# Kernel optimization log

Measured on AMD Instinct MI355X. Metric: run time of the kernel, lower is better.

Reference implementation:

```python
import jax, jax.numpy as jnp
import numpy as np

N_NODES = 100000
N_EDGES = 600000
IN_CH = 128
HID = 128
N_CLASSES = 2
N_GRAPHS = 64


def setup_inputs() -> dict:
    key = jax.random.key(0)
    ks = jax.random.split(key, 12)
    x = jax.random.normal(ks[0], (N_NODES, IN_CH), dtype=jnp.float32)
    edge_index = jax.random.randint(ks[1], (2, N_EDGES), 0, N_NODES, dtype=jnp.int64)
    batch = jnp.sort(jax.random.randint(ks[2], (N_NODES,), 0, N_GRAPHS, dtype=jnp.int64))
    # GCNConv weights (glorot-ish scale) and biases
    def w(k, fan_in, fan_out):
        return jax.random.normal(k, (fan_in, fan_out), dtype=jnp.float32) / np.sqrt(fan_in)
    return {
        "x": x,
        "edge_index": edge_index,
        "batch": batch,
        "W1": w(ks[3], IN_CH, HID), "b1": jnp.zeros((HID,), jnp.float32),
        "W2": w(ks[4], HID, HID), "b2": jnp.zeros((HID,), jnp.float32),
        "W3": w(ks[5], HID, HID), "b3": jnp.zeros((HID,), jnp.float32),
        "Wl": w(ks[6], HID, N_CLASSES), "bl": jnp.zeros((N_CLASSES,), jnp.float32),
    }


def _gcn_conv(x, W, b, row, col, dinv_sqrt):
    # PyG GCNConv: h = x @ W; add self-loops; symmetric norm; scatter-add; + bias
    h = x @ W  # [N, F]
    norm = dinv_sqrt[row] * dinv_sqrt[col]  # [E]
    msg = norm[:, None] * h[row]  # gather + scale, [E, F]
    out = jnp.zeros_like(h).at[col].add(msg)  # scatter-add to destinations
    out = out + (dinv_sqrt * dinv_sqrt)[:, None] * h  # self-loop term (norm = 1/deg)
    return out + b


def reference(x, edge_index, batch, W1, b1, W2, b2, W3, b3, Wl, bl):
    row, col = edge_index[0], edge_index[1]
    # degree with self-loops (in-degree on col, as in PyG default flow)
    deg = jnp.zeros((N_NODES,), jnp.float32).at[col].add(1.0) + 1.0
    dinv_sqrt = jax.lax.rsqrt(deg)

    h = jax.nn.relu(_gcn_conv(x, W1, b1, row, col, dinv_sqrt))
    h = jax.nn.relu(_gcn_conv(h, W2, b2, row, col, dinv_sqrt))
    h = _gcn_conv(h, W3, b3, row, col, dinv_sqrt)

    # global mean pool over graphs
    sums = jax.ops.segment_sum(h, batch, num_segments=N_GRAPHS)  # [G, F]
    counts = jax.ops.segment_sum(jnp.ones((N_NODES,), jnp.float32), batch, num_segments=N_GRAPHS)
    pooled = sums / jnp.maximum(counts, 1.0)[:, None]

    # dropout p=0.0 is identity; final linear head
    return pooled @ Wl + bl
```

## Files before the change

### kernel.cpp

```cpp
#include <hip/hip_runtime.h>

#define NN 100000
#define NE 600000
#define NG 64
#define FD 128
#define NB 98
#define EPAD 1300000
#define GEMM_BLOCKS 512

typedef __attribute__((ext_vector_type(8))) short s8v;
typedef __attribute__((ext_vector_type(4))) float f4v;

__device__ inline float bflo(unsigned u) { return __uint_as_float(u << 16); }
__device__ inline float bfhi(unsigned u) { return __uint_as_float(u & 0xFFFF0000u); }
__device__ inline unsigned f2bfbits(float f) {
  unsigned x = __float_as_uint(f);
  return (x + 0x7FFFu + ((x >> 16) & 1u)) >> 16;
}
__device__ inline unsigned pack2(float a, float b) { return f2bfbits(a) | (f2bfbits(b) << 16); }

__global__ void k_prep(const int* __restrict__ col, int* __restrict__ counts,
                       const float* __restrict__ W1, const float* __restrict__ W2,
                       const float* __restrict__ W3, unsigned short* __restrict__ WTh,
                       unsigned short* __restrict__ WTl, float* __restrict__ psum,
                       const int* __restrict__ batch, int* __restrict__ starts,
                       int* __restrict__ ends) {
  int tid = blockIdx.x * 256 + threadIdx.x;
  if (tid < NE) atomicAdd(&counts[col[tid]], 1);
  if (tid < NG * FD) psum[tid] = 0.f;
  if (tid < 3 * FD * FD) {
    int which = tid / (FD * FD);
    int r = tid - which * (FD * FD);
    const float* W = which == 0 ? W1 : (which == 1 ? W2 : W3);
    int k = r >> 7, n = r & 127;
    float v = W[r];
    unsigned hb = f2bfbits(v);
    float hf = __uint_as_float(hb << 16);
    unsigned lb = f2bfbits(v - hf);
    WTh[which * FD * FD + n * FD + k] = (unsigned short)hb;
    WTl[which * FD * FD + n * FD + k] = (unsigned short)lb;
  }
  int n = tid;
  if (n >= NN) return;
  int g = batch[n];
  if (n == 0) {
    starts[g] = 0;
    for (int q = 0; q < g; ++q) { starts[q] = 0; ends[q] = 0; }
  } else {
    int gp = batch[n - 1];
    if (gp != g) {
      ends[gp] = n;
      starts[g] = n;
      for (int q = gp + 1; q < g; ++q) { starts[q] = n; ends[q] = n; }
    }
  }
  if (n == NN - 1) {
    ends[g] = NN;
    for (int q = g + 1; q < NG; ++q) { starts[q] = NN; ends[q] = NN; }
  }
}

__global__ void k_bsum(const int* __restrict__ counts, int* __restrict__ bsum,
                       float* __restrict__ dinv) {
  __shared__ int wsm[16];
  int b = blockIdx.x, t = threadIdx.x;
  int i = b * 1024 + t;
  int c = (i < NN) ? counts[i] : 0;
  if (i < NN) dinv[i] = rsqrtf((float)c + 1.0f);
  int x = (i < NN) ? ((c + 7) & ~7) : 0;
#pragma unroll
  for (int d = 32; d; d >>= 1) x += __shfl_down(x, d);
  if ((t & 63) == 0) wsm[t >> 6] = x;
  __syncthreads();
  if (t < 16) {
    int s = wsm[t];
#pragma unroll
    for (int d = 8; d; d >>= 1) s += __shfl_down(s, d);
    if (t == 0) bsum[b] = s;
  }
}

__global__ void k_scan2(const int* __restrict__ counts, const int* __restrict__ bsum,
                        int* __restrict__ indptr) {
  __shared__ int wsm[16];
  __shared__ int s_eb;
  int b = blockIdx.x, t = threadIdx.x;
  int i = b * 1024 + t;
  int lane = t & 63, wid = t >> 6;

  if (wid == 0) {
    int s = 0;
    if (lane < NB && lane < b) s += bsum[lane];
    int l2 = lane + 64;
    if (l2 < NB && l2 < b) s += bsum[l2];
#pragma unroll
    for (int d = 32; d; d >>= 1) s += __shfl_down(s, d);
    if (lane == 0) s_eb = s;
  }

  int x = (i < NN) ? ((counts[i] + 7) & ~7) : 0;
  int inc = x;
#pragma unroll
  for (int d = 1; d < 64; d <<= 1) { int y = __shfl_up(inc, d); if (lane >= d) inc += y; }
  if (lane == 63) wsm[wid] = inc;
  __syncthreads();
  if (wid == 0) {
    int s = (lane < 16) ? wsm[lane] : 0;
#pragma unroll
    for (int d = 1; d < 16; d <<= 1) { int y = __shfl_up(s, d); if (lane >= d) s += y; }
    if (lane < 16) wsm[lane] = s;
  }
  __syncthreads();
  int woff = wid ? wsm[wid - 1] : 0;
  if (i < NN) indptr[i + 1] = s_eb + woff + inc;
  if (i == 0) indptr[0] = 0;
}

__global__ void k_fill(const int* __restrict__ row, const int* __restrict__ col,
                       const int* __restrict__ indptr, int* __restrict__ cursor,
                       const int* __restrict__ counts,
                       const float* __restrict__ dinv, uint2* __restrict__ edges) {
  int tid = blockIdx.x * 256 + threadIdx.x;
  if (tid < NN) {
    int base = indptr[tid] + counts[tid];
    int end = indptr[tid + 1];
    for (int p = base; p < end; ++p) edges[p] = make_uint2(0u, 0u);
  }
  if (tid >= NE) return;
  int c = col[tid], r = row[tid];
  int p = indptr[c] + atomicAdd(&cursor[c], 1);
  edges[p] = make_uint2((unsigned)r, __float_as_uint(dinv[r] * dinv[c]));
}

template <int F32A>
__global__ __launch_bounds__(256) void k_gemm(const void* __restrict__ Aab,
                                              const unsigned short* __restrict__ WThi,
                                              const unsigned short* __restrict__ WTlo,
                                              unsigned short* __restrict__ Hb) {
  constexpr int RT = F32A ? 1 : 2;
  constexpr int ROWS = 16 * RT;
  constexpr int NTL = NN / ROWS;
  __shared__ unsigned short wt[256 * 128];
  int t = threadIdx.x, lane = t & 63, w = t >> 6;
  int r16 = lane & 15, kg = lane >> 4;

  {
    const unsigned short* src = (t < 128) ? (WThi + t * FD) : (WTlo + (t - 128) * FD);
#pragma unroll
    for (int j = 0; j < 16; ++j) {
      int ch = j ^ (t & 7);
      *(s8v*)&wt[t * 128 + ch * 8] = *(const s8v*)(src + j * 8);
    }
  }
  __syncthreads();

  const int stride = GEMM_BLOCKS * 4;
  int tile = blockIdx.x * 4 + w;

  float4 aF[8], bF[8], cF[8];
  s8v curB[RT][4], nxtB[RT][4];

  if (F32A) {
    int ld0 = (tile < NTL) ? tile : 0;
    const float* ap = (const float*)Aab + (size_t)(ld0 * 16 + r16) * FD + kg * 8;
#pragma unroll
    for (int c = 0; c < 4; ++c) {
      aF[c * 2] = *(const float4*)(ap + c * 32);
      aF[c * 2 + 1] = *(const float4*)(ap + c * 32 + 4);
    }
    int ld1 = (tile + stride < NTL) ? (tile + stride) : ld0;
    const float* ap1 = (const float*)Aab + (size_t)(ld1 * 16 + r16) * FD + kg * 8;
#pragma unroll
    for (int c = 0; c < 4; ++c) {
      bF[c * 2] = *(const float4*)(ap1 + c * 32);
      bF[c * 2 + 1] = *(const float4*)(ap1 + c * 32 + 4);
    }
  } else {
    if (tile < NTL) {
#pragma unroll
      for (int rt = 0; rt < RT; ++rt) {
        const unsigned short* ap =
            (const unsigned short*)Aab + (size_t)(tile * ROWS + rt * 16 + r16) * FD + kg * 8;
#pragma unroll
        for (int c = 0; c < 4; ++c) curB[rt][c] = *(const s8v*)(ap + c * 32);
      }
    }
  }

  while (tile < NTL) {
    int next = tile + stride;

    {
      if (F32A) {
        int nld = (tile + 2 * stride < NTL) ? (tile + 2 * stride) : tile;
        const float* ap = (const float*)Aab + (size_t)(nld * 16 + r16) * FD + kg * 8;
#pragma unroll
        for (int c = 0; c < 4; ++c) {
          cF[c * 2] = *(const float4*)(ap + c * 32);
          cF[c * 2 + 1] = *(const float4*)(ap + c * 32 + 4);
        }
      } else {
        int nld = (next < NTL) ? next : tile;
#pragma unroll
        for (int rt = 0; rt < RT; ++rt) {
          const unsigned short* ap =
              (const unsigned short*)Aab + (size_t)(nld * ROWS + rt * 16 + r16) * FD + kg * 8;
#pragma unroll
          for (int c = 0; c < 4; ++c) nxtB[rt][c] = *(const s8v*)(ap + c * 32);
        }
      }
    }

    s8v afr[RT][4];
    if (F32A) {
#pragma unroll
      for (int c = 0; c < 4; ++c) {
        float4 p0 = aF[c * 2], p1 = aF[c * 2 + 1];
        s8v f;
        f[0] = (short)f2bfbits(p0.x); f[1] = (short)f2bfbits(p0.y);
        f[2] = (short)f2bfbits(p0.z); f[3] = (short)f2bfbits(p0.w);
        f[4] = (short)f2bfbits(p1.x); f[5] = (short)f2bfbits(p1.y);
        f[6] = (short)f2bfbits(p1.z); f[7] = (short)f2bfbits(p1.w);
        afr[0][c] = f;
      }
    } else {
#pragma unroll
      for (int rt = 0; rt < RT; ++rt)
#pragma unroll
        for (int c = 0; c < 4; ++c) afr[rt][c] = curB[rt][c];
    }

    f4v acc[RT][8];
#pragma unroll
    for (int rt = 0; rt < RT; ++rt)
#pragma unroll
      for (int n = 0; n < 8; ++n) acc[rt][n] = (f4v){0.f, 0.f, 0.f, 0.f};

#pragma unroll
    for (int n = 0; n < 8; ++n) {
      s8v bh[4], bl[4];
#pragma unroll
      for (int c = 0; c < 4; ++c) {
        int ch = (c * 4 + kg) ^ (r16 & 7);
        bh[c] = *(const s8v*)&wt[(n * 16 + r16) * 128 + ch * 8];
        bl[c] = *(const s8v*)&wt[(128 + n * 16 + r16) * 128 + ch * 8];
      }
#pragma unroll
      for (int c = 0; c < 4; ++c)
#pragma unroll
        for (int rt = 0; rt < RT; ++rt)
          acc[rt][n] = __builtin_amdgcn_mfma_f32_16x16x32_bf16(bh[c], afr[rt][c], acc[rt][n], 0, 0, 0);
#pragma unroll
      for (int c = 0; c < 4; ++c)
#pragma unroll
        for (int rt = 0; rt < RT; ++rt)
          acc[rt][n] = __builtin_amdgcn_mfma_f32_16x16x32_bf16(bl[c], afr[rt][c], acc[rt][n], 0, 0, 0);
    }

#pragma unroll
    for (int rt = 0; rt < RT; ++rt) {
      int node = tile * ROWS + rt * 16 + r16;
      unsigned short* hp = Hb + (size_t)node * FD + kg * 4;
#pragma unroll
      for (int n = 0; n < 8; ++n) {
        uint2 v = make_uint2(pack2(acc[rt][n][0], acc[rt][n][1]),
                             pack2(acc[rt][n][2], acc[rt][n][3]));
        *(uint2*)(hp + n * 16) = v;
      }
    }

    if (F32A) {
#pragma unroll
      for (int c = 0; c < 8; ++c) { aF[c] = bF[c]; bF[c] = cF[c]; }
    } else {
#pragma unroll
      for (int rt = 0; rt < RT; ++rt)
#pragma unroll
        for (int c = 0; c < 4; ++c) curB[rt][c] = nxtB[rt][c];
    }
    tile = next;
  }
}

__global__ __launch_bounds__(256) void k_agg(const uint4* __restrict__ H4,
                                             const int* __restrict__ indptr,
                                             const uint4* __restrict__ edges2,
                                             const float* __restrict__ dinv,
                                             const float* __restrict__ bias,
                                             uint4* __restrict__ out4, int relu) {
  int wid = (blockIdx.x * 256 + threadIdx.x) >> 6;
  int ql = threadIdx.x & 15;
  int n = wid * 4 + ((threadIdx.x >> 4) & 3);
  if (n >= NN) return;
  float dv = dinv[n];
  float s2 = dv * dv;
  uint4 u = H4[(size_t)n * 16 + ql];
  float a0 = s2 * bflo(u.x), a1 = s2 * bfhi(u.x);
  float a2 = s2 * bflo(u.y), a3 = s2 * bfhi(u.y);
  float a4 = s2 * bflo(u.z), a5 = s2 * bfhi(u.z);
  float a6 = s2 * bflo(u.w), a7 = s2 * bfhi(u.w);
  int e0 = indptr[n] >> 1, e1 = indptr[n + 1] >> 1;
  for (int e = e0; e < e1; e += 4) {
    uint4 E0 = edges2[e], E1 = edges2[e + 1], E2 = edges2[e + 2], E3 = edges2[e + 3];
    uint4 v0 = H4[(size_t)E0.x * 16 + ql];
    uint4 v1 = H4[(size_t)E0.z * 16 + ql];
    uint4 v2 = H4[(size_t)E1.x * 16 + ql];
    uint4 v3 = H4[(size_t)E1.z * 16 + ql];
    uint4 v4 = H4[(size_t)E2.x * 16 + ql];
    uint4 v5 = H4[(size_t)E2.z * 16 + ql];
    uint4 v6 = H4[(size_t)E3.x * 16 + ql];
    uint4 v7 = H4[(size_t)E3.z * 16 + ql];
    float w0 = __uint_as_float(E0.y), w1 = __uint_as_float(E0.w);
    float w2 = __uint_as_float(E1.y), w3 = __uint_as_float(E1.w);
    float w4 = __uint_as_float(E2.y), w5 = __uint_as_float(E2.w);
    float w6 = __uint_as_float(E3.y), w7 = __uint_as_float(E3.w);
    a0 += w0 * bflo(v0.x); a1 += w0 * bfhi(v0.x); a2 += w0 * bflo(v0.y); a3 += w0 * bfhi(v0.y);
    a4 += w0 * bflo(v0.z); a5 += w0 * bfhi(v0.z); a6 += w0 * bflo(v0.w); a7 += w0 * bfhi(v0.w);
    a0 += w1 * bflo(v1.x); a1 += w1 * bfhi(v1.x); a2 += w1 * bflo(v1.y); a3 += w1 * bfhi(v1.y);
    a4 += w1 * bflo(v1.z); a5 += w1 * bfhi(v1.z); a6 += w1 * bflo(v1.w); a7 += w1 * bfhi(v1.w);
    a0 += w2 * bflo(v2.x); a1 += w2 * bfhi(v2.x); a2 += w2 * bflo(v2.y); a3 += w2 * bfhi(v2.y);
    a4 += w2 * bflo(v2.z); a5 += w2 * bfhi(v2.z); a6 += w2 * bflo(v2.w); a7 += w2 * bfhi(v2.w);
    a0 += w3 * bflo(v3.x); a1 += w3 * bfhi(v3.x); a2 += w3 * bflo(v3.y); a3 += w3 * bfhi(v3.y);
    a4 += w3 * bflo(v3.z); a5 += w3 * bfhi(v3.z); a6 += w3 * bflo(v3.w); a7 += w3 * bfhi(v3.w);
    a0 += w4 * bflo(v4.x); a1 += w4 * bfhi(v4.x); a2 += w4 * bflo(v4.y); a3 += w4 * bfhi(v4.y);
    a4 += w4 * bflo(v4.z); a5 += w4 * bfhi(v4.z); a6 += w4 * bflo(v4.w); a7 += w4 * bfhi(v4.w);
    a0 += w5 * bflo(v5.x); a1 += w5 * bfhi(v5.x); a2 += w5 * bflo(v5.y); a3 += w5 * bfhi(v5.y);
    a4 += w5 * bflo(v5.z); a5 += w5 * bfhi(v5.z); a6 += w5 * bflo(v5.w); a7 += w5 * bfhi(v5.w);
    a0 += w6 * bflo(v6.x); a1 += w6 * bfhi(v6.x); a2 += w6 * bflo(v6.y); a3 += w6 * bfhi(v6.y);
    a4 += w6 * bflo(v6.z); a5 += w6 * bfhi(v6.z); a6 += w6 * bflo(v6.w); a7 += w6 * bfhi(v6.w);
    a0 += w7 * bflo(v7.x); a1 += w7 * bfhi(v7.x); a2 += w7 * bflo(v7.y); a3 += w7 * bfhi(v7.y);
    a4 += w7 * bflo(v7.z); a5 += w7 * bfhi(v7.z); a6 += w7 * bflo(v7.w); a7 += w7 * bfhi(v7.w);
  }
  a0 += bias[ql * 8];     a1 += bias[ql * 8 + 1];
  a2 += bias[ql * 8 + 2]; a3 += bias[ql * 8 + 3];
  a4 += bias[ql * 8 + 4]; a5 += bias[ql * 8 + 5];
  a6 += bias[ql * 8 + 6]; a7 += bias[ql * 8 + 7];
  if (relu) {
    a0 = fmaxf(a0, 0.f); a1 = fmaxf(a1, 0.f); a2 = fmaxf(a2, 0.f); a3 = fmaxf(a3, 0.f);
    a4 = fmaxf(a4, 0.f); a5 = fmaxf(a5, 0.f); a6 = fmaxf(a6, 0.f); a7 = fmaxf(a7, 0.f);
  }
  out4[(size_t)n * 16 + ql] =
      make_uint4(pack2(a0, a1), pack2(a2, a3), pack2(a4, a5), pack2(a6, a7));
}

#define PW 64
__global__ __launch_bounds__(256) void k_pool(const unsigned* __restrict__ H2,
                                              const int* __restrict__ batch,
                                              float* __restrict__ psum) {
  int wgl = (blockIdx.x * 256 + threadIdx.x) >> 6;
  int lane = threadIdx.x & 63;
  int n0 = wgl * PW;
  if (n0 >= NN) return;
  int n1 = n0 + PW; if (n1 > NN) n1 = NN;
  int g0 = batch[n0], g1 = batch[n1 - 1];
  float a0 = 0.f, a1 = 0.f;
  if (g0 == g1) {
    int n = n0;
    for (; n + 3 < n1; n += 4) {
      unsigned v0 = H2[(size_t)(n + 0) * 64 + lane];
      unsigned v1 = H2[(size_t)(n + 1) * 64 + lane];
      unsigned v2 = H2[(size_t)(n + 2) * 64 + lane];
      unsigned v3 = H2[(size_t)(n + 3) * 64 + lane];
      a0 += bflo(v0) + bflo(v1) + bflo(v2) + bflo(v3);
      a1 += bfhi(v0) + bfhi(v1) + bfhi(v2) + bfhi(v3);
    }
    for (; n < n1; ++n) {
      unsigned v = H2[(size_t)n * 64 + lane];
      a0 += bflo(v); a1 += bfhi(v);
    }
    atomicAdd(&psum[g0 * FD + lane * 2], a0);
    atomicAdd(&psum[g0 * FD + lane * 2 + 1], a1);
  } else {
    int g = g0;
    for (int n = n0; n < n1; ++n) {
      int gn = batch[n];
      if (gn != g) {
        atomicAdd(&psum[g * FD + lane * 2], a0);
        atomicAdd(&psum[g * FD + lane * 2 + 1], a1);
        a0 = 0.f; a1 = 0.f; g = gn;
      }
      unsigned v = H2[(size_t)n * 64 + lane];
      a0 += bflo(v); a1 += bfhi(v);
    }
    atomicAdd(&psum[g * FD + lane * 2], a0);
    atomicAdd(&psum[g * FD + lane * 2 + 1], a1);
  }
}

__global__ void k_head(const float* __restrict__ psum, const int* __restrict__ starts,
                       const int* __restrict__ ends, const float* __restrict__ Wl,
                       const float* __restrict__ bl, float* __restrict__ out) {
  int t = threadIdx.x;
  int g = t >> 1, c = t & 1;
  int cnt = ends[g] - starts[g];
  if (cnt < 0) cnt = 0;
  float inv = 1.f / (float)(cnt > 0 ? cnt : 1);
  float acc = 0.f;
  for (int k = 0; k < FD; ++k) acc += psum[g * FD + k] * Wl[k * 2 + c];
  out[g * 2 + c] = acc * inv + bl[c];
}


extern "C" void kernel_launch(void* const* d_in, const int* in_sizes, int n_in,
                              void* d_out, int out_size, void* d_ws, size_t ws_size,
                              hipStream_t stream) {
  const float* x  = (const float*)d_in[0];
  const int* ei   = (const int*)d_in[1];
  const int* bat  = (const int*)d_in[2];
  const float* W1 = (const float*)d_in[3];
  const float* b1 = (const float*)d_in[4];
  const float* W2 = (const float*)d_in[5];
  const float* b2 = (const float*)d_in[6];
  const float* W3 = (const float*)d_in[7];
  const float* b3 = (const float*)d_in[8];
  const float* Wl = (const float*)d_in[9];
  const float* bl = (const float*)d_in[10];
  float* out = (float*)d_out;

  char* ws = (char*)d_ws;
  size_t off = 0;
  auto alloc = [&](size_t bytes) {
    void* p = ws + off;
    off += (bytes + 255) & ~(size_t)255;
    return p;
  };
  int* counts  = (int*)alloc(NN * 4);
  int* cursor  = (int*)alloc(NN * 4);
  int* indptr  = (int*)alloc((NN + 1) * 4);
  float* dinv  = (float*)alloc(NN * 4);
  int* bsum    = (int*)alloc(NB * 4);
  int* starts  = (int*)alloc(NG * 4);
  int* ends    = (int*)alloc(NG * 4);
  float* psum  = (float*)alloc(NG * FD * 4);
  uint2* edges = (uint2*)alloc((size_t)EPAD * 8);
  unsigned short* Hb   = (unsigned short*)alloc((size_t)NN * FD * 2);
  unsigned short* Abuf = (unsigned short*)alloc((size_t)NN * FD * 2);
  unsigned short* WTh  = (unsigned short*)alloc(3 * FD * FD * 2);
  unsigned short* WTl  = (unsigned short*)alloc(3 * FD * FD * 2);

  const int* row = ei;
  const int* col = ei + NE;

  hipMemsetAsync(counts, 0, (size_t)((char*)cursor - (char*)counts) + NN * 4, stream);
  k_prep<<<(NE + 255) / 256, 256, 0, stream>>>(col, counts, W1, W2, W3, WTh, WTl, psum,
                                               bat, starts, ends);
  k_bsum<<<NB, 1024, 0, stream>>>(counts, bsum, dinv);
  k_scan2<<<NB, 1024, 0, stream>>>(counts, bsum, indptr);
  k_fill<<<(NE + 255) / 256, 256, 0, stream>>>(row, col, indptr, cursor, counts, dinv, edges);

  int aggGrid = (NN + 15) / 16;
  int poolGrid = ((NN + PW - 1) / PW * 64 + 255) / 256;

  k_gemm<1><<<GEMM_BLOCKS, 256, 0, stream>>>(x, WTh, WTl, Hb);
  k_agg<<<aggGrid, 256, 0, stream>>>((const uint4*)Hb, indptr, (const uint4*)edges, dinv, b1,
                                     (uint4*)Abuf, 1);
  k_gemm<0><<<GEMM_BLOCKS, 256, 0, stream>>>(Abuf, WTh + FD * FD, WTl + FD * FD, Hb);
  k_agg<<<aggGrid, 256, 0, stream>>>((const uint4*)Hb, indptr, (const uint4*)edges, dinv, b2,
                                     (uint4*)Abuf, 1);
  k_gemm<0><<<GEMM_BLOCKS, 256, 0, stream>>>(Abuf, WTh + 2 * FD * FD, WTl + 2 * FD * FD, Hb);
  k_agg<<<aggGrid, 256, 0, stream>>>((const uint4*)Hb, indptr, (const uint4*)edges, dinv, b3,
                                     (uint4*)Abuf, 0);

  k_pool<<<poolGrid, 256, 0, stream>>>((const unsigned*)Abuf, bat, psum);
  k_head<<<1, 128, 0, stream>>>(psum, starts, ends, Wl, bl, out);
}
```

Measured before the change: 249.8 us.

## Fold last GCN layer and pooling into graph-level aggregation, drop third GEMM

Since the third layer has no activation and is followed by linear mean-pooling and a linear head, the code now pools the normalized adjacency-weighted features directly per graph (Z = P·Â·H2). W3·Wl and b3·Wl are applied only at the end on 64 graph rows. This removes the third full GEMM, the third aggregation pass and its output write, and the separate pool kernel. In exchange, destination graph ids are packed into the upper bits of the edge source index, which caps node ids at 17 bits, and the edge pass flushes per-graph sums with atomics.

Measured after the change: 323.9 us. +29.7%, slower.

```diff
diff --git a/kernel.cpp b/kernel.cpp
--- a/kernel.cpp
+++ b/kernel.cpp
@@ -7,6 +7,7 @@
 #define NB 98
 #define EPAD 1300000
 #define GEMM_BLOCKS 512
+#define SRCM 0x1FFFFu
 
 typedef __attribute__((ext_vector_type(8))) short s8v;
 typedef __attribute__((ext_vector_type(4))) float f4v;
@@ -21,17 +22,16 @@
 
 __global__ void k_prep(const int* __restrict__ col, int* __restrict__ counts,
                        const float* __restrict__ W1, const float* __restrict__ W2,
-                       const float* __restrict__ W3, unsigned short* __restrict__ WTh,
-                       unsigned short* __restrict__ WTl, float* __restrict__ psum,
-                       const int* __restrict__ batch, int* __restrict__ starts,
-                       int* __restrict__ ends) {
+                       unsigned short* __restrict__ WTh, unsigned short* __restrict__ WTl,
+                       float* __restrict__ psum, const int* __restrict__ batch,
+                       int* __restrict__ starts, int* __restrict__ ends) {
   int tid = blockIdx.x * 256 + threadIdx.x;
   if (tid < NE) atomicAdd(&counts[col[tid]], 1);
   if (tid < NG * FD) psum[tid] = 0.f;
-  if (tid < 3 * FD * FD) {
+  if (tid < 2 * FD * FD) {
     int which = tid / (FD * FD);
     int r = tid - which * (FD * FD);
-    const float* W = which == 0 ? W1 : (which == 1 ? W2 : W3);
+    const float* W = which == 0 ? W1 : W2;
     int k = r >> 7, n = r & 127;
     float v = W[r];
     unsigned hb = f2bfbits(v);
@@ -118,18 +118,20 @@
 
 __global__ void k_fill(const int* __restrict__ row, const int* __restrict__ col,
                        const int* __restrict__ indptr, int* __restrict__ cursor,
-                       const int* __restrict__ counts,
+                       const int* __restrict__ counts, const int* __restrict__ batch,
                        const float* __restrict__ dinv, uint2* __restrict__ edges) {
   int tid = blockIdx.x * 256 + threadIdx.x;
   if (tid < NN) {
     int base = indptr[tid] + counts[tid];
     int end = indptr[tid + 1];
-    for (int p = base; p < end; ++p) edges[p] = make_uint2(0u, 0u);
+    unsigned gp = ((unsigned)batch[tid]) << 17;
+    for (int p = base; p < end; ++p) edges[p] = make_uint2(gp, 0u);
   }
   if (tid >= NE) return;
   int c = col[tid], r = row[tid];
   int p = indptr[c] + atomicAdd(&cursor[c], 1);
-  edges[p] = make_uint2((unsigned)r, __float_as_uint(dinv[r] * dinv[c]));
+  unsigned g = ((unsigned)batch[c]) << 17;
+  edges[p] = make_uint2((unsigned)r | g, __float_as_uint(dinv[r] * dinv[c]));
 }
 
 template <int F32A>
@@ -302,14 +304,14 @@
   int e0 = indptr[n] >> 1, e1 = indptr[n + 1] >> 1;
   for (int e = e0; e < e1; e += 4) {
     uint4 E0 = edges2[e], E1 = edges2[e + 1], E2 = edges2[e + 2], E3 = edges2[e + 3];
-    uint4 v0 = H4[(size_t)E0.x * 16 + ql];
-    uint4 v1 = H4[(size_t)E0.z * 16 + ql];
-    uint4 v2 = H4[(size_t)E1.x * 16 + ql];
-    uint4 v3 = H4[(size_t)E1.z * 16 + ql];
-    uint4 v4 = H4[(size_t)E2.x * 16 + ql];
-    uint4 v5 = H4[(size_t)E2.z * 16 + ql];
-    uint4 v6 = H4[(size_t)E3.x * 16 + ql];
-    uint4 v7 = H4[(size_t)E3.z * 16 + ql];
+    uint4 v0 = H4[(size_t)(E0.x & SRCM) * 16 + ql];
+    uint4 v1 = H4[(size_t)(E0.z & SRCM) * 16 + ql];
+    uint4 v2 = H4[(size_t)(E1.x & SRCM) * 16 + ql];
+    uint4 v3 = H4[(size_t)(E1.z & SRCM) * 16 + ql];
+    uint4 v4 = H4[(size_t)(E2.x & SRCM) * 16 + ql];
+    uint4 v5 = H4[(size_t)(E2.z & SRCM) * 16 + ql];
+    uint4 v6 = H4[(size_t)(E3.x & SRCM) * 16 + ql];
+    uint4 v7 = H4[(size_t)(E3.z & SRCM) * 16 + ql];
     float w0 = __uint_as_float(E0.y), w1 = __uint_as_float(E0.w);
     float w2 = __uint_as_float(E1.y), w3 = __uint_as_float(E1.w);
     float w4 = __uint_as_float(E2.y), w5 = __uint_as_float(E2.w);
@@ -343,61 +345,136 @@
       make_uint4(pack2(a0, a1), pack2(a2, a3), pack2(a4, a5), pack2(a6, a7));
 }
 
-#define PW 64
-__global__ __launch_bounds__(256) void k_pool(const unsigned* __restrict__ H2,
+#define ZCH 64
+#define ZNC 16
+#define ZFLUSH(gq)                                                        \
+  {                                                                       \
+    float* zp = &Zg[(gq) * FD + ql * 8];                                  \
+    atomicAdd(zp + 0, a0); atomicAdd(zp + 1, a1);                         \
+    atomicAdd(zp + 2, a2); atomicAdd(zp + 3, a3);                         \
+    atomicAdd(zp + 4, a4); atomicAdd(zp + 5, a5);                         \
+    atomicAdd(zp + 6, a6); atomicAdd(zp + 7, a7);                         \
+  }
+#define ZACCUM(V_, W_)                                                    \
+  {                                                                       \
+    a0 += (W_) * bflo((V_).x); a1 += (W_) * bfhi((V_).x);                 \
+    a2 += (W_) * bflo((V_).y); a3 += (W_) * bfhi((V_).y);                 \
+    a4 += (W_) * bflo((V_).z); a5 += (W_) * bfhi((V_).z);                 \
+    a6 += (W_) * bflo((V_).w); a7 += (W_) * bfhi((V_).w);                 \
+  }
+__global__ __launch_bounds__(256) void k_zacc(const uint4* __restrict__ H4,
+                                              const uint4* __restrict__ edges2,
+                                              const int* __restrict__ indptr,
+                                              const float* __restrict__ dinv,
                                               const int* __restrict__ batch,
-                                              float* __restrict__ psum) {
-  int wgl = (blockIdx.x * 256 + threadIdx.x) >> 6;
-  int lane = threadIdx.x & 63;
-  int n0 = wgl * PW;
-  if (n0 >= NN) return;
-  int n1 = n0 + PW; if (n1 > NN) n1 = NN;
-  int g0 = batch[n0], g1 = batch[n1 - 1];
-  float a0 = 0.f, a1 = 0.f;
-  if (g0 == g1) {
-    int n = n0;
-    for (; n + 3 < n1; n += 4) {
-      unsigned v0 = H2[(size_t)(n + 0) * 64 + lane];
-      unsigned v1 = H2[(size_t)(n + 1) * 64 + lane];
-      unsigned v2 = H2[(size_t)(n + 2) * 64 + lane];
-      unsigned v3 = H2[(size_t)(n + 3) * 64 + lane];
-      a0 += bflo(v0) + bflo(v1) + bflo(v2) + bflo(v3);
-      a1 += bfhi(v0) + bfhi(v1) + bfhi(v2) + bfhi(v3);
-    }
-    for (; n < n1; ++n) {
-      unsigned v = H2[(size_t)n * 64 + lane];
-      a0 += bflo(v); a1 += bfhi(v);
-    }
-    atomicAdd(&psum[g0 * FD + lane * 2], a0);
-    atomicAdd(&psum[g0 * FD + lane * 2 + 1], a1);
-  } else {
-    int g = g0;
+                                              float* __restrict__ Zg) {
+  int qid = (blockIdx.x * 256 + threadIdx.x) >> 4;
+  int ql = threadIdx.x & 15;
+  int nq = (gridDim.x * 256) >> 4;
+  float a0, a1, a2, a3, a4, a5, a6, a7;
+
+  for (int ch = qid; ch < (NN + ZNC - 1) / ZNC; ch += nq) {
+    int n0 = ch * ZNC, n1 = n0 + ZNC;
+    if (n1 > NN) n1 = NN;
+    int g = batch[n0];
+    a0 = a1 = a2 = a3 = a4 = a5 = a6 = a7 = 0.f;
     for (int n = n0; n < n1; ++n) {
       int gn = batch[n];
-      if (gn != g) {
-        atomicAdd(&psum[g * FD + lane * 2], a0);
-        atomicAdd(&psum[g * FD + lane * 2 + 1], a1);
-        a0 = 0.f; a1 = 0.f; g = gn;
-      }
-      unsigned v = H2[(size_t)n * 64 + lane];
-      a0 += bflo(v); a1 += bfhi(v);
-    }
-    atomicAdd(&psum[g * FD + lane * 2], a0);
-    atomicAdd(&psum[g * FD + lane * 2 + 1], a1);
-  }
-}
-
-__global__ void k_head(const float* __restrict__ psum, const int* __restrict__ starts,
-                       const int* __restrict__ ends, const float* __restrict__ Wl,
-                       const float* __restrict__ bl, float* __restrict__ out) {
+      if (gn != g) { ZFLUSH(g); a0 = a1 = a2 = a3 = a4 = a5 = a6 = a7 = 0.f; g = gn; }
+      float dv = dinv[n];
+      float wq = dv * dv;
+      uint4 v = H4[(size_t)n * 16 + ql];
+      ZACCUM(v, wq);
+    }
+    ZFLUSH(g);
+  }
+
+  int totPairs = indptr[NN] >> 1;
+  for (int ch = qid; ch < (totPairs + ZCH - 1) / ZCH; ch += nq) {
+    int e0 = ch * ZCH, e1 = e0 + ZCH;
+    if (e1 > totPairs) e1 = totPairs;
+    int g = (int)(edges2[e0].x >> 17);
+    a0 = a1 = a2 = a3 = a4 = a5 = a6 = a7 = 0.f;
+    int e = e0;
+    while (e < e1) {
+      if (e + 3 < e1) {
+        uint4 E0 = edges2[e], E1 = edges2[e + 1], E2 = edges2[e + 2], E3 = edges2[e + 3];
+        unsigned gg = (E0.x >> 17) | (E0.z >> 17) | (E1.x >> 17) | (E1.z >> 17) |
+                      (E2.x >> 17) | (E2.z >> 17) | (E3.x >> 17) | (E3.z >> 17);
+        unsigned ga = (E0.x >> 17) & (E0.z >> 17) & (E1.x >> 17) & (E1.z >> 17) &
+                      (E2.x >> 17) & (E2.z >> 17) & (E3.x >> 17) & (E3.z >> 17);
+        if (gg == (unsigned)g && ga == (unsigned)g) {
+          uint4 v0 = H4[(size_t)(E0.x & SRCM) * 16 + ql];
+          uint4 v1 = H4[(size_t)(E0.z & SRCM) * 16 + ql];
+          uint4 v2 = H4[(size_t)(E1.x & SRCM) * 16 + ql];
+          uint4 v3 = H4[(size_t)(E1.z & SRCM) * 16 + ql];
+          uint4 v4 = H4[(size_t)(E2.x & SRCM) * 16 + ql];
+          uint4 v5 = H4[(size_t)(E2.z & SRCM) * 16 + ql];
+          uint4 v6 = H4[(size_t)(E3.x & SRCM) * 16 + ql];
+          uint4 v7 = H4[(size_t)(E3.z & SRCM) * 16 + ql];
+          float w0 = __uint_as_float(E0.y), w1 = __uint_as_float(E0.w);
+          float w2 = __uint_as_float(E1.y), w3 = __uint_as_float(E1.w);
+          float w4 = __uint_as_float(E2.y), w5 = __uint_as_float(E2.w);
+          float w6 = __uint_as_float(E3.y), w7 = __uint_as_float(E3.w);
+          ZACCUM(v0, w0); ZACCUM(v1, w1);
+          ZACCUM(v2, w2); ZACCUM(v3, w3);
+          ZACCUM(v4, w4); ZACCUM(v5, w5);
+          ZACCUM(v6, w6); ZACCUM(v7, w7);
+          e += 4;
+          continue;
+        }
+      }
+      uint4 E = edges2[e];
+      int g0 = (int)(E.x >> 17);
+      if (g0 != g) { ZFLUSH(g); a0 = a1 = a2 = a3 = a4 = a5 = a6 = a7 = 0.f; g = g0; }
+      {
+        uint4 v = H4[(size_t)(E.x & SRCM) * 16 + ql];
+        float wq = __uint_as_float(E.y);
+        ZACCUM(v, wq);
+      }
+      int g1 = (int)(E.z >> 17);
+      if (g1 != g) { ZFLUSH(g); a0 = a1 = a2 = a3 = a4 = a5 = a6 = a7 = 0.f; g = g1; }
+      {
+        uint4 v = H4[(size_t)(E.z & SRCM) * 16 + ql];
+        float wq = __uint_as_float(E.w);
+        ZACCUM(v, wq);
+      }
+      ++e;
+    }
+    ZFLUSH(g);
+  }
+}
+
+__global__ void k_head2(const float* __restrict__ Z, const int* __restrict__ starts,
+                        const int* __restrict__ ends, const float* __restrict__ W3,
+                        const float* __restrict__ Wl, const float* __restrict__ b3,
+                        const float* __restrict__ bl, float* __restrict__ out) {
+  __shared__ float w3wl[FD][2];
+  __shared__ float b3wl[2];
   int t = threadIdx.x;
+  {
+    float s0 = 0.f, s1 = 0.f;
+    for (int o = 0; o < FD; ++o) {
+      float w = W3[t * FD + o];
+      s0 += w * Wl[o * 2];
+      s1 += w * Wl[o * 2 + 1];
+    }
+    w3wl[t][0] = s0;
+    w3wl[t][1] = s1;
+  }
+  if (t < 2) {
+    float s = 0.f;
+    for (int o = 0; o < FD; ++o) s += b3[o] * Wl[o * 2 + t];
+    b3wl[t] = s;
+  }
+  __syncthreads();
   int g = t >> 1, c = t & 1;
   int cnt = ends[g] - starts[g];
   if (cnt < 0) cnt = 0;
   float inv = 1.f / (float)(cnt > 0 ? cnt : 1);
   float acc = 0.f;
-  for (int k = 0; k < FD; ++k) acc += psum[g * FD + k] * Wl[k * 2 + c];
-  out[g * 2 + c] = acc * inv + bl[c];
+  for (int k = 0; k < FD; ++k) acc += Z[g * FD + k] * w3wl[k][c];
+  out[g * 2 + c] = acc * inv + (cnt > 0 ? b3wl[c] : 0.f) + bl[c];
 }
 
 
@@ -435,21 +512,21 @@
   uint2* edges = (uint2*)alloc((size_t)EPAD * 8);
   unsigned short* Hb   = (unsigned short*)alloc((size_t)NN * FD * 2);
   unsigned short* Abuf = (unsigned short*)alloc((size_t)NN * FD * 2);
-  unsigned short* WTh  = (unsigned short*)alloc(3 * FD * FD * 2);
-  unsigned short* WTl  = (unsigned short*)alloc(3 * FD * FD * 2);
+  unsigned short* WTh  = (unsigned short*)alloc(2 * FD * FD * 2);
+  unsigned short* WTl  = (unsigned short*)alloc(2 * FD * FD * 2);
 
   const int* row = ei;
   const int* col = ei + NE;
 
   hipMemsetAsync(counts, 0, (size_t)((char*)cursor - (char*)counts) + NN * 4, stream);
-  k_prep<<<(NE + 255) / 256, 256, 0, stream>>>(col, counts, W1, W2, W3, WTh, WTl, psum,
+  k_prep<<<(NE + 255) / 256, 256, 0, stream>>>(col, counts, W1, W2, WTh, WTl, psum,
                                                bat, starts, ends);
   k_bsum<<<NB, 1024, 0, stream>>>(counts, bsum, dinv);
   k_scan2<<<NB, 1024, 0, stream>>>(counts, bsum, indptr);
-  k_fill<<<(NE + 255) / 256, 256, 0, stream>>>(row, col, indptr, cursor, counts, dinv, edges);
+  k_fill<<<(NE + 255) / 256, 256, 0, stream>>>(row, col, indptr, cursor, counts, bat,
+                                               dinv, edges);
 
   int aggGrid = (NN + 15) / 16;
-  int poolGrid = ((NN + PW - 1) / PW * 64 + 255) / 256;
 
   k_gemm<1><<<GEMM_BLOCKS, 256, 0, stream>>>(x, WTh, WTl, Hb);
   k_agg<<<aggGrid, 256, 0, stream>>>((const uint4*)Hb, indptr, (const uint4*)edges, dinv, b1,
@@ -457,10 +534,7 @@
   k_gemm<0><<<GEMM_BLOCKS, 256, 0, stream>>>(Abuf, WTh + FD * FD, WTl + FD * FD, Hb);
   k_agg<<<aggGrid, 256, 0, stream>>>((const uint4*)Hb, indptr, (const uint4*)edges, dinv, b2,
                                      (uint4*)Abuf, 1);
-  k_gemm<0><<<GEMM_BLOCKS, 256, 0, stream>>>(Abuf, WTh + 2 * FD * FD, WTl + 2 * FD * FD, Hb);
-  k_agg<<<aggGrid, 256, 0, stream>>>((const uint4*)Hb, indptr, (const uint4*)edges, dinv, b3,
-                                     (uint4*)Abuf, 0);
-
-  k_pool<<<poolGrid, 256, 0, stream>>>((const unsigned*)Abuf, bat, psum);
-  k_head<<<1, 128, 0, stream>>>(psum, starts, ends, Wl, bl, out);
-}
+  k_zacc<<<1024, 256, 0, stream>>>((const uint4*)Abuf, (const uint4*)edges, indptr, dinv,
+                                   bat, psum);
+  k_head2<<<1, 128, 0, stream>>>(psum, starts, ends, W3, Wl, b3, bl, out);
+}
```
